# Kernel tuning notes

Hardware: AMD Instinct MI355X
Metric: run time of the kernel (lower is better)

## Reference

```python
import jax, jax.numpy as jnp
import numpy as np

N_NODES = 50000
N_EDGES = 800000
IN_FEATS = 256
NUM_HEADS = 8
OUT_FEATS = 32
NEG_SLOPE = 0.2


def setup_inputs() -> dict:
    key = jax.random.key(0)
    ks = jax.random.split(key, 10)
    feat = jax.random.normal(ks[0], (N_NODES, IN_FEATS), dtype=jnp.float32)
    edge_emb = jax.random.normal(ks[1], (N_EDGES, NUM_HEADS), dtype=jnp.float32)
    src = jax.random.randint(ks[2], (N_EDGES,), 0, N_NODES, dtype=jnp.int32)
    dst = jax.random.randint(ks[3], (N_EDGES,), 0, N_NODES, dtype=jnp.int32)
    # learned params (xavier-style scale)
    W_src = jax.random.normal(ks[4], (IN_FEATS, NUM_HEADS * OUT_FEATS), dtype=jnp.float32) * 0.05
    W_e = jax.random.normal(ks[5], (NUM_HEADS, NUM_HEADS * OUT_FEATS), dtype=jnp.float32) * 0.3
    attn_l = jax.random.normal(ks[6], (NUM_HEADS, OUT_FEATS), dtype=jnp.float32) * 0.2
    attn_r = jax.random.normal(ks[7], (NUM_HEADS, OUT_FEATS), dtype=jnp.float32) * 0.2
    attn_e = jax.random.normal(ks[8], (NUM_HEADS, OUT_FEATS), dtype=jnp.float32) * 0.2
    bias = jnp.zeros((NUM_HEADS * OUT_FEATS,), dtype=jnp.float32)
    return {"feat": feat, "edge_emb": edge_emb, "src": src, "dst": dst,
            "W_src": W_src, "W_e": W_e, "attn_l": attn_l, "attn_r": attn_r,
            "attn_e": attn_e, "bias": bias}


def reference(feat, edge_emb, src, dst, W_src, W_e, attn_l, attn_r, attn_e, bias):
    N = feat.shape[0]
    H, D = attn_l.shape
    # node projections (share_weights=True -> fc_dst is fc_src)
    h = (feat @ W_src).reshape(N, H, D)            # (N, H, D)
    ef = (edge_emb @ W_e).reshape(-1, H, D)        # (E, H, D)
    # per-head attention scalars
    el = jnp.einsum("nhd,hd->nh", h, attn_l)      # (N, H)
    er = jnp.einsum("nhd,hd->nh", h, attn_r)      # (N, H)
    ee = jnp.einsum("ehd,hd->eh", ef, attn_e)     # (E, H)
    logits = jax.nn.leaky_relu(el[src] + er[dst] + ee, NEG_SLOPE)  # (E, H)
    # edge softmax over incoming edges of each dst node (numerically stable)
    m = jax.ops.segment_max(logits, dst, num_segments=N)
    m = jnp.where(jnp.isfinite(m), m, 0.0)
    p = jnp.exp(logits - m[dst])
    s = jax.ops.segment_sum(p, dst, num_segments=N)
    alpha = p / (s[dst] + 1e-9)                    # (E, H)
    # weighted message aggregation
    out = jax.ops.segment_sum(alpha[:, :, None] * h[src], dst, num_segments=N)  # (N, H, D)
    out = out + bias.reshape(1, H, D)
    return out
```

## Files before the change

kernel.cpp:

```cpp
#include <hip/hip_runtime.h>

#define H 8
#define D 32
#define HD 256
#define NEG_SLOPE 0.2f
#define SCB 1024

typedef __attribute__((ext_vector_type(8))) short bf8;
typedef __attribute__((ext_vector_type(4))) float f4;

__device__ __forceinline__ unsigned short f2b(float x) {
    unsigned u = __float_as_uint(x);
    unsigned r = (u + 0x7fffu + ((u >> 16) & 1u)) >> 16;
    return (unsigned short)r;
}

__global__ __launch_bounds__(256) void k_prep(
        const float* __restrict__ W, unsigned short* __restrict__ Wtb,
        const float* __restrict__ W_e, const float* __restrict__ attn_e,
        float* __restrict__ M, const int* __restrict__ dst, int* __restrict__ cnt,
        int* __restrict__ ord, int E, int bh) {
    const int b = blockIdx.x, t = threadIdx.x;
    if (b < HD) {
        Wtb[b * HD + t] = f2b(W[t * HD + b]);
    } else if (b < HD + bh) {
        int e = (b - HD) * 256 + t;
        if (e < E) ord[e] = atomicAdd(&cnt[dst[e]], 1);
    } else {
        if (t < 64) {
            int k = t >> 3, hh = t & 7;
            float acc = 0.f;
            for (int d = 0; d < D; ++d)
                acc = fmaf(W_e[k * HD + hh * D + d], attn_e[hh * D + d], acc);
            M[k * 8 + hh] = acc;
        }
    }
}

__global__ __launch_bounds__(1024) void k_scan1(const int* __restrict__ cnt,
                                                int* __restrict__ offs,
                                                int* __restrict__ btot, int N) {
    __shared__ int wtot[16], wbase[16];
    const int t = threadIdx.x, wid = t >> 6, lane = t & 63;
    int i = blockIdx.x * SCB + t;
    int v = (i < N) ? cnt[i] : 0;
    int x = v;
#pragma unroll
    for (int off = 1; off < 64; off <<= 1) {
        int y = __shfl_up(x, off, 64);
        if (lane >= off) x += y;
    }
    if (lane == 63) wtot[wid] = x;
    __syncthreads();
    if (t < 16) {
        int w = wtot[t], xs = w;
#pragma unroll
        for (int off = 1; off < 16; off <<= 1) {
            int y = __shfl_up(xs, off, 64);
            if (t >= off) xs += y;
        }
        wbase[t] = xs - w;
        if (t == 15) btot[blockIdx.x] = xs;
    }
    __syncthreads();
    if (i < N) offs[i] = wbase[wid] + (x - v);
}

__global__ __launch_bounds__(1024) void k_scan3(int* __restrict__ offs,
                                                const int* __restrict__ btot,
                                                int N, int E, int nb) {
    __shared__ int bb;
    const int t = threadIdx.x;
    if (t < 64) {
        int vv = (t < nb) ? btot[t] : 0;
        int x = vv;
#pragma unroll
        for (int off = 1; off < 64; off <<= 1) {
            int y = __shfl_up(x, off, 64);
            if (t >= off) x += y;
        }
        if (t == blockIdx.x) bb = x - vv;
    }
    __syncthreads();
    const int i = blockIdx.x * SCB + t;
    if (i < N) offs[i] += bb;
    if (i == 0) offs[N] = E;
}

__global__ __launch_bounds__(256) void k_fuse(
        const float* __restrict__ feat, const unsigned short* __restrict__ Wtb,
        const float* __restrict__ attn_l, const float* __restrict__ attn_r,
        unsigned short* __restrict__ hb, float* __restrict__ el,
        float* __restrict__ er, int N, int bg,
        const int* __restrict__ src, const int* __restrict__ dst,
        const int* __restrict__ offs, const int* __restrict__ ord,
        uint2* __restrict__ pair, int E) {
    const int t = threadIdx.x;
    if (blockIdx.x >= bg) {
        int e = (blockIdx.x - bg) * 256 + t;
        if (e < E) {
            int p = offs[dst[e]] + ord[e];
            pair[p] = make_uint2((unsigned)src[e], (unsigned)e);
        }
        return;
    }
    const int l = t & 63, wv = t >> 6;
    const int row0 = (blockIdx.x * 4 + wv) * 16;
    if (row0 >= N) return;
    const int m = l & 15, q = l >> 4;

    bf8 afr[8];
    const float* arow = feat + (size_t)(row0 + m) * HD + q * 8;
#pragma unroll
    for (int kc = 0; kc < 8; ++kc) {
        const float4 f0 = *(const float4*)(arow + kc * 32);
        const float4 f1 = *(const float4*)(arow + kc * 32 + 4);
        bf8 a;
        a[0] = (short)f2b(f0.x); a[1] = (short)f2b(f0.y);
        a[2] = (short)f2b(f0.z); a[3] = (short)f2b(f0.w);
        a[4] = (short)f2b(f1.x); a[5] = (short)f2b(f1.y);
        a[6] = (short)f2b(f1.z); a[7] = (short)f2b(f1.w);
        afr[kc] = a;
    }

    f4 acc[16];
#pragma unroll
    for (int nt = 0; nt < 16; ++nt) acc[nt] = (f4){0.f, 0.f, 0.f, 0.f};

    const unsigned short* bcol = Wtb + (size_t)m * HD + q * 8;
#pragma unroll
    for (int nt = 0; nt < 16; ++nt) {
        const unsigned short* bp = bcol + (size_t)nt * 16 * HD;
#pragma unroll
        for (int kc = 0; kc < 8; ++kc) {
            const bf8 b = *(const bf8*)(bp + kc * 32);
            acc[nt] = __builtin_amdgcn_mfma_f32_16x16x32_bf16(afr[kc], b, acc[nt], 0, 0, 0);
        }
    }

#pragma unroll
    for (int h = 0; h < H; ++h) {
        float elp[4] = {0.f, 0.f, 0.f, 0.f};
        float erp[4] = {0.f, 0.f, 0.f, 0.f};
#pragma unroll
        for (int s = 0; s < 2; ++s) {
            const int nt = h * 2 + s;
            const int c = nt * 16 + m;
            const float alc = attn_l[c];
            const float arc = attn_r[c];
#pragma unroll
            for (int reg = 0; reg < 4; ++reg) {
                const float v = acc[nt][reg];
                hb[(size_t)(row0 + q * 4 + reg) * HD + c] = f2b(v);
                elp[reg] = fmaf(v, alc, elp[reg]);
                erp[reg] = fmaf(v, arc, erp[reg]);
            }
        }
#pragma unroll
        for (int reg = 0; reg < 4; ++reg) {
#pragma unroll
            for (int off = 1; off < 16; off <<= 1) {
                elp[reg] += __shfl_xor(elp[reg], off, 16);
                erp[reg] += __shfl_xor(erp[reg], off, 16);
            }
        }
        if (m == 0) {
#pragma unroll
            for (int reg = 0; reg < 4; ++reg) {
                el[(row0 + q * 4 + reg) * H + h] = elp[reg];
                er[(row0 + q * 4 + reg) * H + h] = erp[reg];
            }
        }
    }
}

__global__ __launch_bounds__(256) void k_node(
        const int* __restrict__ offs, const uint2* __restrict__ pair,
        const float* __restrict__ edge_emb, const float* __restrict__ el,
        const float* __restrict__ er, const float* __restrict__ M,
        const unsigned short* __restrict__ hb, const float* __restrict__ bias,
        float* __restrict__ out, int N) {
    const int t = threadIdx.x;
    const int lane = t & 63;
    const int v = blockIdx.x * 4 + (t >> 6);
    if (v >= N) return;
    const int hh = lane & 7;
    const int sl = lane & 31;
    const int half = lane >> 5;
    const int cb = sl * 8;
    const int hq = sl >> 2;
    const int s0 = offs[v];
    const int deg = offs[v + 1] - s0;

    float Mreg[8];
#pragma unroll
    for (int k = 0; k < 8; ++k) Mreg[k] = M[k * 8 + hh];
    const float erv = er[(size_t)v * 8 + hh];
    const unsigned short* hbc = hb + cb;

    float a[8];
#pragma unroll
    for (int i = 0; i < 8; ++i) a[i] = 0.f;
    float psum = 0.f;

    for (int j0 = 0; j0 < deg; j0 += 64) {
        const int nj = min(64, deg - j0);
        uint2 prl = make_uint2(0u, 0u);
        if (lane < nj) prl = pair[s0 + j0 + lane];

        float pv[8];
#pragma unroll
        for (int s = 0; s < 8; ++s) {
            pv[s] = 0.f;
            if (s * 8 < nj) {
                const int j = s * 8 + (lane >> 3);
                const unsigned sx = __shfl(prl.x, j, 64);
                const unsigned ex = __shfl(prl.y, j, 64);
                const float eev = edge_emb[(size_t)ex * 8 + hh];
                float lg = el[(size_t)sx * 8 + hh] + erv;
#pragma unroll
                for (int k = 0; k < 8; ++k)
                    lg = fmaf(__shfl(eev, k, 8), Mreg[k], lg);
                lg = (lg >= 0.f) ? lg : NEG_SLOPE * lg;
                if (j < nj) { pv[s] = __expf(lg); psum += pv[s]; }
            }
        }

#pragma unroll
        for (int s = 0; s < 8; ++s) {
            if (s * 8 >= nj) break;
#pragma unroll
            for (int u = 0; u < 4; ++u) {
                if (s * 8 + 2 * u >= nj) break;
                const int jj = 2 * u + half;
                const unsigned sx = __shfl(prl.x, s * 8 + jj, 64);
                const float pj = __shfl(pv[s], jj * 8 + hq, 64);
                const uint4 w = *(const uint4*)(hbc + (size_t)sx * HD);
                a[0] = fmaf(pj, __uint_as_float(w.x << 16), a[0]);
                a[1] = fmaf(pj, __uint_as_float(w.x & 0xffff0000u), a[1]);
                a[2] = fmaf(pj, __uint_as_float(w.y << 16), a[2]);
                a[3] = fmaf(pj, __uint_as_float(w.y & 0xffff0000u), a[3]);
                a[4] = fmaf(pj, __uint_as_float(w.z << 16), a[4]);
                a[5] = fmaf(pj, __uint_as_float(w.z & 0xffff0000u), a[5]);
                a[6] = fmaf(pj, __uint_as_float(w.w << 16), a[6]);
                a[7] = fmaf(pj, __uint_as_float(w.w & 0xffff0000u), a[7]);
            }
        }
    }

#pragma unroll
    for (int i = 0; i < 8; ++i) a[i] += __shfl_xor(a[i], 32, 64);

    psum += __shfl_xor(psum, 8, 64);
    psum += __shfl_xor(psum, 16, 64);
    psum += __shfl_xor(psum, 32, 64);
    const float rs = 1.f / (__shfl(psum, hq, 8) + 1e-9f);
    if (half == 0) {
        const float4 b0 = *(const float4*)&bias[cb];
        const float4 b1 = *(const float4*)&bias[cb + 4];
        *(float4*)&out[(size_t)v * HD + cb] =
            make_float4(fmaf(a[0], rs, b0.x), fmaf(a[1], rs, b0.y),
                        fmaf(a[2], rs, b0.z), fmaf(a[3], rs, b0.w));
        *(float4*)&out[(size_t)v * HD + cb + 4] =
            make_float4(fmaf(a[4], rs, b1.x), fmaf(a[5], rs, b1.y),
                        fmaf(a[6], rs, b1.z), fmaf(a[7], rs, b1.w));
    }
}

extern "C" void kernel_launch(void* const* d_in, const int* in_sizes, int n_in,
                              void* d_out, int out_size, void* d_ws, size_t ws_size,
                              hipStream_t stream) {
    const float* feat     = (const float*)d_in[0];
    const float* edge_emb = (const float*)d_in[1];
    const int*   src      = (const int*)d_in[2];
    const int*   dst      = (const int*)d_in[3];
    const float* W_src    = (const float*)d_in[4];
    const float* W_e      = (const float*)d_in[5];
    const float* attn_l   = (const float*)d_in[6];
    const float* attn_r   = (const float*)d_in[7];
    const float* attn_e   = (const float*)d_in[8];
    const float* bias     = (const float*)d_in[9];
    float* out = (float*)d_out;

    const int N = in_sizes[0] / HD;
    const int E = in_sizes[2];

    char* ws = (char*)d_ws;
    unsigned short* hb = (unsigned short*)ws; ws += (size_t)N * HD * 2;
    uint2* pair = (uint2*)ws; ws += (size_t)E * 8;
    float* el   = (float*)ws; ws += (size_t)N * H * 4;
    float* er   = (float*)ws; ws += (size_t)N * H * 4;
    int*   cnt  = (int*)ws;   ws += (size_t)N * 4;
    int* offs   = (int*)ws; ws += (size_t)(N + 1) * 4;
    int* ord    = (int*)ws; ws += (size_t)E * 4;
    unsigned short* Wtb = (unsigned short*)ws; ws += (size_t)HD * HD * 2;
    int* btot  = (int*)ws; ws += 64 * 4;
    float* M   = (float*)ws; ws += 256;

    const int bh  = (E + 255) / 256;
    const int nsb = (N + SCB - 1) / SCB;
    const int bg  = ((N + 15) / 16 + 3) / 4;
    const int bs  = (E + 255) / 256;

    hipMemsetAsync(cnt, 0, (size_t)N * 4, stream);
    k_prep  <<<HD + bh + 1, 256, 0, stream>>>(W_src, Wtb, W_e, attn_e, M,
                                              dst, cnt, ord, E, bh);
    k_scan1 <<<nsb, SCB, 0, stream>>>(cnt, offs, btot, N);
    k_scan3 <<<nsb, SCB, 0, stream>>>(offs, btot, N, E, nsb);
    k_fuse  <<<bg + bs, 256, 0, stream>>>(feat, Wtb, attn_l, attn_r, hb, el, er,
                                          N, bg, src, dst, offs, ord, pair, E);
    k_node  <<<(N + 3) / 4, 256, 0, stream>>>(offs, pair, edge_emb, el, er, M,
                                              hb, bias, out, N);
}
```

Measured before the change: 334.9 us.

## Stage projection weights in swizzled LDS and widen fused GEMM blocks

The fused projection kernel now uses 512-thread blocks that cover 8 row tiles. Each block stages the bf16 weight matrix into shared memory in two 64KB halves with an XOR swizzle, so the MFMA B operands come from LDS rather than from per-wave global loads. The edge-scatter part also processes 2048 edges per block with a strided loop. This cuts redundant global/L2 traffic for the weights, but adds two barriers, 64KB of LDS per block (which limits occupancy), and the extra time to fill the shared buffer.

Result: faster. 296.6 us (-11.4%).

```diff
diff --git a/kernel.cpp b/kernel.cpp
--- a/kernel.cpp
+++ b/kernel.cpp
@@ -87,7 +87,7 @@
     if (i == 0) offs[N] = E;
 }
 
-__global__ __launch_bounds__(256) void k_fuse(
+__global__ __launch_bounds__(512) void k_fuse(
         const float* __restrict__ feat, const unsigned short* __restrict__ Wtb,
         const float* __restrict__ attn_l, const float* __restrict__ attn_r,
         unsigned short* __restrict__ hb, float* __restrict__ el,
@@ -97,46 +97,68 @@
         uint2* __restrict__ pair, int E) {
     const int t = threadIdx.x;
     if (blockIdx.x >= bg) {
-        int e = (blockIdx.x - bg) * 256 + t;
-        if (e < E) {
+        const int base = (blockIdx.x - bg) * 2048;
+        const int end = min(base + 2048, E);
+        for (int e = base + t; e < end; e += 512) {
             int p = offs[dst[e]] + ord[e];
             pair[p] = make_uint2((unsigned)src[e], (unsigned)e);
         }
         return;
     }
+    __shared__ unsigned short lwt[128 * HD];
     const int l = t & 63, wv = t >> 6;
-    const int row0 = (blockIdx.x * 4 + wv) * 16;
-    if (row0 >= N) return;
+    const int row0 = (blockIdx.x * 8 + wv) * 16;
+    const bool act = row0 < N;
     const int m = l & 15, q = l >> 4;
 
     bf8 afr[8];
-    const float* arow = feat + (size_t)(row0 + m) * HD + q * 8;
-#pragma unroll
-    for (int kc = 0; kc < 8; ++kc) {
-        const float4 f0 = *(const float4*)(arow + kc * 32);
-        const float4 f1 = *(const float4*)(arow + kc * 32 + 4);
-        bf8 a;
-        a[0] = (short)f2b(f0.x); a[1] = (short)f2b(f0.y);
-        a[2] = (short)f2b(f0.z); a[3] = (short)f2b(f0.w);
-        a[4] = (short)f2b(f1.x); a[5] = (short)f2b(f1.y);
-        a[6] = (short)f2b(f1.z); a[7] = (short)f2b(f1.w);
-        afr[kc] = a;
+    if (act) {
+        const float* arow = feat + (size_t)(row0 + m) * HD + q * 8;
+#pragma unroll
+        for (int kc = 0; kc < 8; ++kc) {
+            const float4 f0 = *(const float4*)(arow + kc * 32);
+            const float4 f1 = *(const float4*)(arow + kc * 32 + 4);
+            bf8 a;
+            a[0] = (short)f2b(f0.x); a[1] = (short)f2b(f0.y);
+            a[2] = (short)f2b(f0.z); a[3] = (short)f2b(f0.w);
+            a[4] = (short)f2b(f1.x); a[5] = (short)f2b(f1.y);
+            a[6] = (short)f2b(f1.z); a[7] = (short)f2b(f1.w);
+            afr[kc] = a;
+        }
     }
 
     f4 acc[16];
 #pragma unroll
     for (int nt = 0; nt < 16; ++nt) acc[nt] = (f4){0.f, 0.f, 0.f, 0.f};
 
-    const unsigned short* bcol = Wtb + (size_t)m * HD + q * 8;
-#pragma unroll
-    for (int nt = 0; nt < 16; ++nt) {
-        const unsigned short* bp = bcol + (size_t)nt * 16 * HD;
-#pragma unroll
-        for (int kc = 0; kc < 8; ++kc) {
-            const bf8 b = *(const bf8*)(bp + kc * 32);
-            acc[nt] = __builtin_amdgcn_mfma_f32_16x16x32_bf16(afr[kc], b, acc[nt], 0, 0, 0);
-        }
-    }
+    const uint4* wt4 = (const uint4*)Wtb;
+    uint4* l4 = (uint4*)lwt;
+#pragma unroll
+    for (int half = 0; half < 2; ++half) {
+        if (half) __syncthreads();
+#pragma unroll
+        for (int i = 0; i < 8; ++i) {
+            const int u = i * 512 + t;
+            l4[u ^ ((u >> 5) & 7)] = wt4[half * 4096 + u];
+        }
+        __syncthreads();
+        if (act) {
+#pragma unroll
+            for (int ntl = 0; ntl < 8; ++ntl) {
+                const int nt = half * 8 + ntl;
+                const int lc = ntl * 16 + m;
+                const unsigned short* bp = lwt + lc * HD;
+                const int sw = (lc & 7) * 8;
+#pragma unroll
+                for (int kc = 0; kc < 8; ++kc) {
+                    const bf8 b = *(const bf8*)(bp + ((q * 8 + kc * 32) ^ sw));
+                    acc[nt] = __builtin_amdgcn_mfma_f32_16x16x32_bf16(
+                                  afr[kc], b, acc[nt], 0, 0, 0);
+                }
+            }
+        }
+    }
+    if (!act) return;
 
 #pragma unroll
     for (int h = 0; h < H; ++h) {
@@ -299,15 +321,15 @@
 
     const int bh  = (E + 255) / 256;
     const int nsb = (N + SCB - 1) / SCB;
-    const int bg  = ((N + 15) / 16 + 3) / 4;
-    const int bs  = (E + 255) / 256;
+    const int bg  = ((N + 15) / 16 + 7) / 8;
+    const int bs  = (E + 2047) / 2048;
 
     hipMemsetAsync(cnt, 0, (size_t)N * 4, stream);
     k_prep  <<<HD + bh + 1, 256, 0, stream>>>(W_src, Wtb, W_e, attn_e, M,
                                               dst, cnt, ord, E, bh);
     k_scan1 <<<nsb, SCB, 0, stream>>>(cnt, offs, btot, N);
     k_scan3 <<<nsb, SCB, 0, stream>>>(offs, btot, N, E, nsb);
-    k_fuse  <<<bg + bs, 256, 0, stream>>>(feat, Wtb, attn_l, attn_r, hb, el, er,
+    k_fuse  <<<bg + bs, 512, 0, stream>>>(feat, Wtb, attn_l, attn_r, hb, el, er,
                                           N, bg, src, dst, offs, ord, pair, E);
     k_node  <<<(N + 3) / 4, 256, 0, stream>>>(offs, pair, edge_emb, el, er, M,
                                               hb, bias, out, N);
```
